# Performance work log

Measured on AMD Instinct MI355X. Metric: run time of the kernel, lower is better.

The kernel has to match this reference:

```python
import jax, jax.numpy as jnp
import numpy as np

WIDTH = 256
HEAD = 16
SCALE = 2
G = WIDTH // HEAD          # 16 groups
NH = G * SCALE             # 32 kernelized heads
EPS = 1e-5
N_NODES = 20000
B_GRAPHS = 1024


def setup_inputs() -> dict:
    key = jax.random.key(0)
    ks = jax.random.split(key, 10)
    x = jax.random.normal(ks[0], (N_NODES, WIDTH), jnp.float32)
    x_res = jax.random.normal(ks[1], (B_GRAPHS, NH, HEAD, HEAD), jnp.float32)
    batch = jnp.sort(jax.random.randint(ks[2], (N_NODES,), 0, B_GRAPHS)).astype(jnp.int64)
    w_pre = jax.random.normal(ks[3], (WIDTH, WIDTH), jnp.float32) * 0.02
    b_pre = jnp.zeros((WIDTH,), jnp.float32)
    # grouped 1x1 convs: [groups, width_scale, head_out, head_in]
    wq = jax.random.normal(ks[4], (G, SCALE, HEAD, HEAD), jnp.float32) * 0.02
    wk = jax.random.normal(ks[5], (G, SCALE, HEAD, HEAD), jnp.float32) * 0.02
    wv = jax.random.normal(ks[6], (G, SCALE, HEAD, HEAD), jnp.float32) * 0.02
    w_post = jax.random.normal(ks[7], (WIDTH, WIDTH * SCALE), jnp.float32) * 0.02
    b_post = jnp.zeros((WIDTH,), jnp.float32)
    log_scale = jnp.full((WIDTH,), np.log(0.01), jnp.float32)
    return {"x": x, "x_res": x_res, "batch": batch, "batch_size": B_GRAPHS,
            "w_pre": w_pre, "b_pre": b_pre, "wq": wq, "wk": wk, "wv": wv,
            "w_post": w_post, "b_post": b_post, "log_scale": log_scale}


def reference(x, x_res, batch, batch_size, w_pre, b_pre, wq, wk, wv, w_post, b_post, log_scale):
    n = x.shape[0]
    # pre: 1x1 conv (= linear) + GroupNorm(affine=False); L=1 so normalize over
    # each group's width_head channels.
    y = x @ w_pre.T + b_pre                       # [N, width]
    yg = y.reshape(n, G, HEAD)                    # [N, G, Hd]
    mu = yg.mean(-1, keepdims=True)
    var = yg.var(-1, keepdims=True)               # biased, as in GroupNorm
    yn = (yg - mu) / jnp.sqrt(var + EPS)          # [N, G, Hd]

    inv_sqrt_h = 1.0 / np.sqrt(HEAD)
    # grouped convs -> kernelized q,k (exp) and v
    xq = jnp.exp(jnp.einsum('ngi,gsoi->ngso', yn, wq) * inv_sqrt_h).reshape(n, NH, HEAD)
    xk = jnp.exp(jnp.einsum('ngi,gsoi->ngso', yn, wk) * inv_sqrt_h).reshape(n, NH, HEAD)
    xv = jnp.einsum('ngi,gsoi->ngso', yn, wv).reshape(n, NH, HEAD)

    # outer product k (x) v then scatter-sum over graphs  [B, NH, Hd, Hd]
    kv = jnp.einsum('bnh,bnv->bnhv', xk, xv)
    kv_sum = jax.ops.segment_sum(kv, batch, num_segments=batch_size) + x_res
    x_res_out = kv_sum

    # per-graph key sum, gathered back to nodes
    k_sum = jax.ops.segment_sum(xk, batch, num_segments=batch_size)[batch]  # [N, NH, Hd]
    denom = jnp.einsum('bnh,bnh->bn', xq, k_sum)                            # [N, NH]
    qn = xq / denom[:, :, None]

    out = jnp.einsum('bnh,bnhv->bnv', qn, kv_sum[batch]).reshape(n, WIDTH * SCALE)
    out = jnp.exp(log_scale) * (out @ w_post.T + b_post)                    # [N, width]
    return (out, x_res_out)
```

## Files before the change

kernel.cpp:

```cpp
#include <hip/hip_runtime.h>
#include <stdint.h>

typedef unsigned int u32;
typedef unsigned short u16;
typedef __attribute__((ext_vector_type(8))) short v8s;
typedef __attribute__((ext_vector_type(4))) float v4f;

#define GN_EPS 1e-5f

__device__ __forceinline__ float bflo(u32 u){ return __uint_as_float(u << 16); }
__device__ __forceinline__ float bfhi(u32 u){ return __uint_as_float(u & 0xffff0000u); }
__device__ __forceinline__ u16 f2bf(float f){
  u32 x = __float_as_uint(f);
  u32 r = (x + 0x7fffu + ((x >> 16) & 1u)) >> 16;
  return (u16)r;
}
__device__ __forceinline__ u32 pack2(float a, float b){
  return (u32)f2bf(a) | ((u32)f2bf(b) << 16);
}
__device__ __forceinline__ void unpack8(const uint4 u, float* f){
  f[0]=bflo(u.x); f[1]=bfhi(u.x); f[2]=bflo(u.y); f[3]=bfhi(u.y);
  f[4]=bflo(u.z); f[5]=bfhi(u.z); f[6]=bflo(u.w); f[7]=bfhi(u.w);
}
__device__ __forceinline__ uint4 loadpack8(const float* __restrict__ p){
  float4 a = *(const float4*)p, b = *(const float4*)(p + 4);
  return make_uint4(pack2(a.x,a.y),pack2(a.z,a.w),pack2(b.x,b.y),pack2(b.z,b.w));
}

__device__ __forceinline__ int getb(const int* __restrict__ b, int is64, int i){
  return b[is64 ? 2*i : i];
}

__global__ __launch_bounds__(256) void k_detect(
    const int* __restrict__ batch, int n, int* __restrict__ flags)
{
  int i = blockIdx.x*256 + threadIdx.x;
  int bad = 0;
  if (i < n - 1 && batch[i] > batch[i + 1]) bad = 1;
  if (__builtin_amdgcn_ballot_w64(bad) != 0 && (threadIdx.x & 63) == 0)
    atomicOr(&flags[0], 1);
}

__global__ __launch_bounds__(256) void k_pre(
    const float* __restrict__ x, const float* __restrict__ wpre,
    const float* __restrict__ bpre, float* __restrict__ y, int N, int nbm)
{
  __shared__ __align__(16) u16 As[64*40];
  __shared__ __align__(16) u16 Bs[64*40];
  const int t = threadIdx.x;
  const int bm = blockIdx.x % nbm;
  const int bn = blockIdx.x / nbm;
  const int m_base = bm*64, n_base = bn*64;
  const int w = t >> 6, lane = t & 63;
  const int wm = (w >> 1)*32, wn = (w & 1)*32;
  const int fr = lane & 15, fk = lane >> 4;
  const int srow = t >> 2, scol = (t & 3)*8;

  v4f acc[2][2];
#pragma unroll
  for (int i = 0; i < 2; i++)
#pragma unroll
    for (int j = 0; j < 2; j++) acc[i][j] = (v4f){0.f,0.f,0.f,0.f};

  for (int k0 = 0; k0 < 256; k0 += 32) {
    __syncthreads();
    {
      int gm = m_base + srow;
      uint4 av = make_uint4(0u,0u,0u,0u);
      if (gm < N) av = loadpack8(x + (size_t)gm*256 + k0 + scol);
      *(uint4*)&As[srow*40 + scol] = av;
      uint4 bv = loadpack8(wpre + (size_t)(n_base + srow)*256 + k0 + scol);
      *(uint4*)&Bs[srow*40 + scol] = bv;
    }
    __syncthreads();
    v8s a0 = *(const v8s*)&As[(wm      + fr)*40 + fk*8];
    v8s a1 = *(const v8s*)&As[(wm + 16 + fr)*40 + fk*8];
    v8s b0 = *(const v8s*)&Bs[(wn      + fr)*40 + fk*8];
    v8s b1 = *(const v8s*)&Bs[(wn + 16 + fr)*40 + fk*8];
    acc[0][0] = __builtin_amdgcn_mfma_f32_16x16x32_bf16(a0,b0,acc[0][0],0,0,0);
    acc[0][1] = __builtin_amdgcn_mfma_f32_16x16x32_bf16(a0,b1,acc[0][1],0,0,0);
    acc[1][0] = __builtin_amdgcn_mfma_f32_16x16x32_bf16(a1,b0,acc[1][0],0,0,0);
    acc[1][1] = __builtin_amdgcn_mfma_f32_16x16x32_bf16(a1,b1,acc[1][1],0,0,0);
  }
#pragma unroll
  for (int nj = 0; nj < 2; nj++) {
    int col = n_base + wn + nj*16 + fr;
    float bpv = bpre[col];
#pragma unroll
    for (int mi = 0; mi < 2; mi++) {
#pragma unroll
      for (int r = 0; r < 4; r++) {
        int row = m_base + wm + mi*16 + fk*4 + r;
        if (row < N) y[(size_t)row*256 + col] = acc[mi][nj][r] + bpv;
      }
    }
  }
}

__global__ __launch_bounds__(256) void k_gnqkv(
    const float* __restrict__ y, const float* __restrict__ wq,
    const float* __restrict__ wk, const float* __restrict__ wv,
    u16* __restrict__ qo, u16* __restrict__ ko, u16* __restrict__ vo, int N)
{
  __shared__ __align__(16) float wL[3*512];
  const int t = threadIdx.x;
  const int g = blockIdx.x & 15;
  const int c = blockIdx.x >> 4;
  {
    const float* srcs[3] = {wq, wk, wv};
#pragma unroll
    for (int tz = 0; tz < 3; tz++) {
      wL[tz*512 + t]       = srcs[tz][g*512 + t];
      wL[tz*512 + t + 256] = srcs[tz][g*512 + t + 256];
    }
  }
  __syncthreads();
  const int node = c*256 + t;
  if (node >= N) return;

  const float* yp = y + (size_t)node*256 + g*16;
  float4 v0 = *(const float4*)yp;
  float4 v1 = *(const float4*)(yp + 4);
  float4 v2 = *(const float4*)(yp + 8);
  float4 v3 = *(const float4*)(yp + 12);
  float a[16] = {v0.x,v0.y,v0.z,v0.w, v1.x,v1.y,v1.z,v1.w,
                 v2.x,v2.y,v2.z,v2.w, v3.x,v3.y,v3.z,v3.w};
  float mu = 0.f;
#pragma unroll
  for (int i = 0; i < 16; i++) mu += a[i];
  mu *= 0.0625f;
  float s2 = 0.f;
#pragma unroll
  for (int i = 0; i < 16; i++) { float d = a[i]-mu; s2 = fmaf(d,d,s2); }
  float inv = rsqrtf(s2*0.0625f + GN_EPS);
  float yn[16];
#pragma unroll
  for (int i = 0; i < 16; i++) yn[i] = (a[i]-mu)*inv;

  u16* outs[3] = {qo, ko, vo};
#pragma unroll
  for (int tz = 0; tz < 3; tz++) {
#pragma unroll
    for (int s = 0; s < 2; s++) {
      u32 p[8];
#pragma unroll
      for (int o = 0; o < 16; o++) {
        const float* row = &wL[tz*512 + (s*16 + o)*16];
        float4 W0 = *(const float4*)row;
        float4 W1 = *(const float4*)(row + 4);
        float4 W2 = *(const float4*)(row + 8);
        float4 W3 = *(const float4*)(row + 12);
        float w[16] = {W0.x,W0.y,W0.z,W0.w,W1.x,W1.y,W1.z,W1.w,
                       W2.x,W2.y,W2.z,W2.w,W3.x,W3.y,W3.z,W3.w};
        float d = 0.f;
#pragma unroll
        for (int i = 0; i < 16; i++) d = fmaf(yn[i], w[i], d);
        if (tz < 2) d = __expf(d*0.25f);
        if (o & 1) p[o>>1] |= (u32)f2bf(d) << 16;
        else       p[o>>1]  = (u32)f2bf(d);
      }
      u16* dst = outs[tz] + (size_t)node*512 + g*32 + s*16;
      *(uint4*)dst       = make_uint4(p[0],p[1],p[2],p[3]);
      *(uint4*)(dst + 8) = make_uint4(p[4],p[5],p[6],p[7]);
    }
  }
}

__device__ __forceinline__ int lbound(const int* __restrict__ a, int is64,
                                      int lo, int n, int key){
  int l = lo, h = n;
  while (l < h) { int m = (l + h) >> 1; if (getb(a, is64, m) < key) l = m + 1; else h = m; }
  return l;
}

__global__ __launch_bounds__(256) void k_segatt(
    const u16* __restrict__ xk, const u16* __restrict__ xv,
    const u16* __restrict__ xq, const float* __restrict__ xres,
    const int* __restrict__ batch, const int* __restrict__ flags,
    float* __restrict__ out1, u16* __restrict__ att, int N)
{
  __shared__ float ksh[4][512];
  __shared__ float vsh[4][512];
  __shared__ __align__(16) float kvs[32*258];
  __shared__ __align__(16) float kss[32*17];
  const int b = blockIdx.x, t = threadIdx.x;
  const int is64 = flags[0];
  const int lo = lbound(batch, is64, 0, N, b);
  const int hi = lbound(batch, is64, lo, N, b + 1);

  float kv[2][16];
#pragma unroll
  for (int r = 0; r < 2; r++)
#pragma unroll
    for (int v = 0; v < 16; v++) kv[r][v] = 0.f;
  float ks0 = 0.f, ks1 = 0.f;
  const int nh = t >> 3, hp = t & 7;

  for (int base = lo; base < hi; base += 4) {
    __syncthreads();
    {
      int j = t >> 6, e8 = (t & 63)*8;
      uint4 K4 = make_uint4(0u,0u,0u,0u), V4 = make_uint4(0u,0u,0u,0u);
      int node = base + j;
      if (node < hi) {
        K4 = *(const uint4*)(xk + (size_t)node*512 + e8);
        V4 = *(const uint4*)(xv + (size_t)node*512 + e8);
      }
      float kf[8], vf[8]; unpack8(K4, kf); unpack8(V4, vf);
#pragma unroll
      for (int i = 0; i < 8; i++) { ksh[j][e8+i] = kf[i]; vsh[j][e8+i] = vf[i]; }
    }
    __syncthreads();
#pragma unroll
    for (int j = 0; j < 4; j++) {
      float k0 = ksh[j][nh*16 + 2*hp], k1 = ksh[j][nh*16 + 2*hp + 1];
      float4 V0 = *(const float4*)&vsh[j][nh*16];
      float4 V1 = *(const float4*)&vsh[j][nh*16 + 4];
      float4 V2 = *(const float4*)&vsh[j][nh*16 + 8];
      float4 V3 = *(const float4*)&vsh[j][nh*16 + 12];
      float vv[16] = {V0.x,V0.y,V0.z,V0.w,V1.x,V1.y,V1.z,V1.w,
                      V2.x,V2.y,V2.z,V2.w,V3.x,V3.y,V3.z,V3.w};
#pragma unroll
      for (int v = 0; v < 16; v++) {
        kv[0][v] = fmaf(k0, vv[v], kv[0][v]);
        kv[1][v] = fmaf(k1, vv[v], kv[1][v]);
      }
      ks0 += ksh[j][2*t]; ks1 += ksh[j][2*t + 1];
    }
  }
  kss[nh*17 + 2*hp]     = ks0;
  kss[nh*17 + 2*hp + 1] = ks1;

#pragma unroll
  for (int r = 0; r < 2; r++) {
    int h = 2*hp + r;
    size_t idx = ((size_t)(b*32 + nh)*16 + h)*16;
    const float* xp = xres + idx;
    float4 X0 = *(const float4*)xp;
    float4 X1 = *(const float4*)(xp + 4);
    float4 X2 = *(const float4*)(xp + 8);
    float4 X3 = *(const float4*)(xp + 12);
    float xf[16] = {X0.x,X0.y,X0.z,X0.w,X1.x,X1.y,X1.z,X1.w,
                    X2.x,X2.y,X2.z,X2.w,X3.x,X3.y,X3.z,X3.w};
    float o[16];
#pragma unroll
    for (int j = 0; j < 16; j++) o[j] = kv[r][j] + xf[j];
    float* op = out1 + idx;
    *(float4*)op        = make_float4(o[0],o[1],o[2],o[3]);
    *(float4*)(op + 4)  = make_float4(o[4],o[5],o[6],o[7]);
    *(float4*)(op + 8)  = make_float4(o[8],o[9],o[10],o[11]);
    *(float4*)(op + 12) = make_float4(o[12],o[13],o[14],o[15]);
    float* lp = &kvs[nh*258 + h*16];
#pragma unroll
    for (int j = 0; j < 8; j++)
      *(float2*)&lp[2*j] = make_float2(o[2*j], o[2*j+1]);
  }
  __syncthreads();

  const int nh2 = t & 31, ns = t >> 5;
  for (int n0 = lo; n0 < hi; n0 += 8) {
    int node = n0 + ns;
    if (node >= hi) continue;
    const u16* qp = xq + (size_t)node*512 + nh2*16;
    uint4 Q0 = *(const uint4*)qp;
    uint4 Q1 = *(const uint4*)(qp + 8);
    float q[16]; unpack8(Q0, q); unpack8(Q1, q + 8);
    const float* ksp = &kss[nh2*17];
    float denom = 0.f;
#pragma unroll
    for (int i = 0; i < 16; i++) denom = fmaf(q[i], ksp[i], denom);
    float inv = 1.0f / fmaxf(denom, 1e-20f);
    float a[16];
#pragma unroll
    for (int v = 0; v < 16; v++) a[v] = 0.f;
    const float* kvp = &kvs[nh2*258];
#pragma unroll
    for (int h = 0; h < 16; h++) {
      float qh = q[h] * inv;
#pragma unroll
      for (int j = 0; j < 8; j++) {
        float2 w = *(const float2*)&kvp[h*16 + 2*j];
        a[2*j]   = fmaf(qh, w.x, a[2*j]);
        a[2*j+1] = fmaf(qh, w.y, a[2*j+1]);
      }
    }
    u32 p[8];
#pragma unroll
    for (int j = 0; j < 8; j++) p[j] = pack2(a[2*j], a[2*j+1]);
    u16* dst = att + (size_t)node*512 + nh2*16;
    *(uint4*)dst       = make_uint4(p[0],p[1],p[2],p[3]);
    *(uint4*)(dst + 8) = make_uint4(p[4],p[5],p[6],p[7]);
  }
}

__global__ __launch_bounds__(256) void k_post(
    const u16* __restrict__ att, const float* __restrict__ wpost,
    const float* __restrict__ bpost, const float* __restrict__ ls,
    float* __restrict__ out0, int N, int nbm)
{
  __shared__ __align__(16) u16 As[64*40];
  __shared__ __align__(16) u16 Bs[64*40];
  const int t = threadIdx.x;
  const int bm = blockIdx.x % nbm;
  const int bn = blockIdx.x / nbm;
  const int m_base = bm*64, n_base = bn*64;
  const int w = t >> 6, lane = t & 63;
  const int wm = (w >> 1)*32, wn = (w & 1)*32;
  const int fr = lane & 15, fk = lane >> 4;
  const int srow = t >> 2, scol = (t & 3)*8;

  v4f acc[2][2];
#pragma unroll
  for (int i = 0; i < 2; i++)
#pragma unroll
    for (int j = 0; j < 2; j++) acc[i][j] = (v4f){0.f,0.f,0.f,0.f};

  for (int k0 = 0; k0 < 512; k0 += 32) {
    __syncthreads();
    {
      int gm = m_base + srow;
      uint4 av = make_uint4(0u,0u,0u,0u);
      if (gm < N) av = *(const uint4*)(att + (size_t)gm*512 + k0 + scol);
      *(uint4*)&As[srow*40 + scol] = av;
      uint4 bv = loadpack8(wpost + (size_t)(n_base + srow)*512 + k0 + scol);
      *(uint4*)&Bs[srow*40 + scol] = bv;
    }
    __syncthreads();
    v8s a0 = *(const v8s*)&As[(wm      + fr)*40 + fk*8];
    v8s a1 = *(const v8s*)&As[(wm + 16 + fr)*40 + fk*8];
    v8s b0 = *(const v8s*)&Bs[(wn      + fr)*40 + fk*8];
    v8s b1 = *(const v8s*)&Bs[(wn + 16 + fr)*40 + fk*8];
    acc[0][0] = __builtin_amdgcn_mfma_f32_16x16x32_bf16(a0,b0,acc[0][0],0,0,0);
    acc[0][1] = __builtin_amdgcn_mfma_f32_16x16x32_bf16(a0,b1,acc[0][1],0,0,0);
    acc[1][0] = __builtin_amdgcn_mfma_f32_16x16x32_bf16(a1,b0,acc[1][0],0,0,0);
    acc[1][1] = __builtin_amdgcn_mfma_f32_16x16x32_bf16(a1,b1,acc[1][1],0,0,0);
  }
#pragma unroll
  for (int nj = 0; nj < 2; nj++) {
    int col = n_base + wn + nj*16 + fr;
    float bpv = bpost[col];
    float e   = __expf(ls[col]);
#pragma unroll
    for (int mi = 0; mi < 2; mi++) {
#pragma unroll
      for (int r = 0; r < 4; r++) {
        int row = m_base + wm + mi*16 + fk*4 + r;
        if (row < N) out0[(size_t)row*256 + col] = e*(acc[mi][nj][r] + bpv);
      }
    }
  }
}

extern "C" void kernel_launch(void* const* d_in, const int* in_sizes, int n_in,
                              void* d_out, int out_size, void* d_ws, size_t ws_size,
                              hipStream_t stream)
{
  const float* x     = (const float*)d_in[0];
  const float* xres  = (const float*)d_in[1];
  const int*   batch = (const int*)d_in[2];
  const float* wpre  = (const float*)d_in[4];
  const float* bpre  = (const float*)d_in[5];
  const float* wq    = (const float*)d_in[6];
  const float* wk    = (const float*)d_in[7];
  const float* wv    = (const float*)d_in[8];
  const float* wpost = (const float*)d_in[9];
  const float* bpost = (const float*)d_in[10];
  const float* ls    = (const float*)d_in[11];

  const int N = in_sizes[0] / 256;
  const int B = in_sizes[1] / 8192;
  const int nbm = (N + 63) / 64;
  const int nchunk = (N + 255) / 256;

  char* ws = (char*)d_ws;
  size_t off = 0;
  int*   flags = (int*)(ws + off); off += 256;
  float* y     = (float*)(ws + off);
  u16*   att   = (u16*)(ws + off);  off += (size_t)N * 1024;
  u16*   q     = (u16*)(ws + off);  off += (size_t)N * 1024;
  u16*   kten  = (u16*)(ws + off);  off += (size_t)N * 1024;
  u16*   vten  = (u16*)(ws + off);  off += (size_t)N * 1024;

  float* out0 = (float*)d_out;
  float* out1 = out0 + (size_t)N * 256;

  hipMemsetAsync(flags, 0, 4, stream);
  k_detect<<<nchunk,         256, 0, stream>>>(batch, N, flags);
  k_pre   <<<nbm * 4,        256, 0, stream>>>(x, wpre, bpre, y, N, nbm);
  k_gnqkv <<<nchunk * 16,    256, 0, stream>>>(y, wq, wk, wv, q, kten, vten, N);
  k_segatt<<<B,              256, 0, stream>>>(kten, vten, q, xres, batch, flags,
                                               out1, att, N);
  k_post  <<<nbm * 4,        256, 0, stream>>>(att, wpost, bpost, ls, out0, N, nbm);
}
```

Before: 138.4 us.

## Precompute segment bounds and stream K/V directly from global in segatt

Adds a kernel that computes per-graph start offsets once, replacing the two binary searches each segatt block ran over the batch array. The K/V accumulation loop drops the LDS staging and per-4-node barriers, so each thread now reads its own K pair and V row straight from global memory, node by node. The combined kv tile held in LDS is stored as bf16 instead of fp32, which cuts LDS footprint and may raise occupancy, but adds rounding to the att computation. It also adds one extra kernel launch, and the direct global loads are redundant across threads, so they rely on cache hits.

Measured after the change: 135.9 us. About the same (-1.8%).

```diff
diff --git a/kernel.cpp b/kernel.cpp
--- a/kernel.cpp
+++ b/kernel.cpp
@@ -39,6 +39,20 @@
   if (i < n - 1 && batch[i] > batch[i + 1]) bad = 1;
   if (__builtin_amdgcn_ballot_w64(bad) != 0 && (threadIdx.x & 63) == 0)
     atomicOr(&flags[0], 1);
+}
+
+__global__ __launch_bounds__(256) void k_bounds(
+    const int* __restrict__ batch, const int* __restrict__ flags,
+    int N, int B, int* __restrict__ bounds)
+{
+  int i = blockIdx.x*256 + threadIdx.x;
+  if (i >= N) return;
+  const int is64 = flags[0];
+  int b = getb(batch, is64, i);
+  int prev = (i == 0) ? -1 : getb(batch, is64, i - 1);
+  for (int g = prev + 1; g <= b; g++) bounds[g] = i;
+  if (i == N - 1)
+    for (int g = b + 1; g <= B; g++) bounds[g] = N;
 }
 
 __global__ __launch_bounds__(256) void k_pre(
@@ -166,27 +180,17 @@
   }
 }
 
-__device__ __forceinline__ int lbound(const int* __restrict__ a, int is64,
-                                      int lo, int n, int key){
-  int l = lo, h = n;
-  while (l < h) { int m = (l + h) >> 1; if (getb(a, is64, m) < key) l = m + 1; else h = m; }
-  return l;
-}
-
 __global__ __launch_bounds__(256) void k_segatt(
     const u16* __restrict__ xk, const u16* __restrict__ xv,
     const u16* __restrict__ xq, const float* __restrict__ xres,
-    const int* __restrict__ batch, const int* __restrict__ flags,
+    const int* __restrict__ bounds,
     float* __restrict__ out1, u16* __restrict__ att, int N)
 {
-  __shared__ float ksh[4][512];
-  __shared__ float vsh[4][512];
-  __shared__ __align__(16) float kvs[32*258];
-  __shared__ __align__(16) float kss[32*17];
+  __shared__ __align__(16) u16 kvs[32*280];
+  __shared__ float kss[32*17];
   const int b = blockIdx.x, t = threadIdx.x;
-  const int is64 = flags[0];
-  const int lo = lbound(batch, is64, 0, N, b);
-  const int hi = lbound(batch, is64, lo, N, b + 1);
+  const int lo = bounds[b], hi = bounds[b+1];
+  const int nh = t >> 3, hp = t & 7;
 
   float kv[2][16];
 #pragma unroll
@@ -194,38 +198,20 @@
 #pragma unroll
     for (int v = 0; v < 16; v++) kv[r][v] = 0.f;
   float ks0 = 0.f, ks1 = 0.f;
-  const int nh = t >> 3, hp = t & 7;
-
-  for (int base = lo; base < hi; base += 4) {
-    __syncthreads();
-    {
-      int j = t >> 6, e8 = (t & 63)*8;
-      uint4 K4 = make_uint4(0u,0u,0u,0u), V4 = make_uint4(0u,0u,0u,0u);
-      int node = base + j;
-      if (node < hi) {
-        K4 = *(const uint4*)(xk + (size_t)node*512 + e8);
-        V4 = *(const uint4*)(xv + (size_t)node*512 + e8);
-      }
-      float kf[8], vf[8]; unpack8(K4, kf); unpack8(V4, vf);
-#pragma unroll
-      for (int i = 0; i < 8; i++) { ksh[j][e8+i] = kf[i]; vsh[j][e8+i] = vf[i]; }
-    }
-    __syncthreads();
-#pragma unroll
-    for (int j = 0; j < 4; j++) {
-      float k0 = ksh[j][nh*16 + 2*hp], k1 = ksh[j][nh*16 + 2*hp + 1];
-      float4 V0 = *(const float4*)&vsh[j][nh*16];
-      float4 V1 = *(const float4*)&vsh[j][nh*16 + 4];
-      float4 V2 = *(const float4*)&vsh[j][nh*16 + 8];
-      float4 V3 = *(const float4*)&vsh[j][nh*16 + 12];
-      float vv[16] = {V0.x,V0.y,V0.z,V0.w,V1.x,V1.y,V1.z,V1.w,
-                      V2.x,V2.y,V2.z,V2.w,V3.x,V3.y,V3.z,V3.w};
-#pragma unroll
-      for (int v = 0; v < 16; v++) {
-        kv[0][v] = fmaf(k0, vv[v], kv[0][v]);
-        kv[1][v] = fmaf(k1, vv[v], kv[1][v]);
-      }
-      ks0 += ksh[j][2*t]; ks1 += ksh[j][2*t + 1];
+
+  const size_t koff = (size_t)nh*16 + 2*hp;
+  const size_t voff = (size_t)nh*16;
+  for (int node = lo; node < hi; node++) {
+    u32 kw = *(const u32*)(xk + (size_t)node*512 + koff);
+    uint4 V0 = *(const uint4*)(xv + (size_t)node*512 + voff);
+    uint4 V1 = *(const uint4*)(xv + (size_t)node*512 + voff + 8);
+    float k0 = bflo(kw), k1 = bfhi(kw);
+    float vf[16]; unpack8(V0, vf); unpack8(V1, vf + 8);
+    ks0 += k0; ks1 += k1;
+#pragma unroll
+    for (int v = 0; v < 16; v++) {
+      kv[0][v] = fmaf(k0, vf[v], kv[0][v]);
+      kv[1][v] = fmaf(k1, vf[v], kv[1][v]);
     }
   }
   kss[nh*17 + 2*hp]     = ks0;
@@ -250,10 +236,11 @@
     *(float4*)(op + 4)  = make_float4(o[4],o[5],o[6],o[7]);
     *(float4*)(op + 8)  = make_float4(o[8],o[9],o[10],o[11]);
     *(float4*)(op + 12) = make_float4(o[12],o[13],o[14],o[15]);
-    float* lp = &kvs[nh*258 + h*16];
-#pragma unroll
-    for (int j = 0; j < 8; j++)
-      *(float2*)&lp[2*j] = make_float2(o[2*j], o[2*j+1]);
+    u16* lp = &kvs[nh*280 + h*16];
+    *(uint4*)lp       = make_uint4(pack2(o[0],o[1]),  pack2(o[2],o[3]),
+                                   pack2(o[4],o[5]),  pack2(o[6],o[7]));
+    *(uint4*)(lp + 8) = make_uint4(pack2(o[8],o[9]),  pack2(o[10],o[11]),
+                                   pack2(o[12],o[13]),pack2(o[14],o[15]));
   }
   __syncthreads();
 
@@ -273,16 +260,15 @@
     float a[16];
 #pragma unroll
     for (int v = 0; v < 16; v++) a[v] = 0.f;
-    const float* kvp = &kvs[nh2*258];
+    const u16* kvp = &kvs[nh2*280];
 #pragma unroll
     for (int h = 0; h < 16; h++) {
       float qh = q[h] * inv;
-#pragma unroll
-      for (int j = 0; j < 8; j++) {
-        float2 w = *(const float2*)&kvp[h*16 + 2*j];
-        a[2*j]   = fmaf(qh, w.x, a[2*j]);
-        a[2*j+1] = fmaf(qh, w.y, a[2*j+1]);
-      }
+      uint4 W0 = *(const uint4*)(kvp + h*16);
+      uint4 W1 = *(const uint4*)(kvp + h*16 + 8);
+      float w[16]; unpack8(W0, w); unpack8(W1, w + 8);
+#pragma unroll
+      for (int v = 0; v < 16; v++) a[v] = fmaf(qh, w[v], a[v]);
     }
     u32 p[8];
 #pragma unroll
@@ -374,21 +360,23 @@
 
   char* ws = (char*)d_ws;
   size_t off = 0;
-  int*   flags = (int*)(ws + off); off += 256;
-  float* y     = (float*)(ws + off);
-  u16*   att   = (u16*)(ws + off);  off += (size_t)N * 1024;
-  u16*   q     = (u16*)(ws + off);  off += (size_t)N * 1024;
-  u16*   kten  = (u16*)(ws + off);  off += (size_t)N * 1024;
-  u16*   vten  = (u16*)(ws + off);  off += (size_t)N * 1024;
+  int*   flags  = (int*)(ws + off); off += 256;
+  int*   bounds = (int*)(ws + off); off += ((size_t)B + 64) * 4;
+  float* y      = (float*)(ws + off);
+  u16*   att    = (u16*)(ws + off);  off += (size_t)N * 1024;
+  u16*   q      = (u16*)(ws + off);  off += (size_t)N * 1024;
+  u16*   kten   = (u16*)(ws + off);  off += (size_t)N * 1024;
+  u16*   vten   = (u16*)(ws + off);  off += (size_t)N * 1024;
 
   float* out0 = (float*)d_out;
   float* out1 = out0 + (size_t)N * 256;
 
   hipMemsetAsync(flags, 0, 4, stream);
   k_detect<<<nchunk,         256, 0, stream>>>(batch, N, flags);
+  k_bounds<<<nchunk,         256, 0, stream>>>(batch, flags, N, B, bounds);
   k_pre   <<<nbm * 4,        256, 0, stream>>>(x, wpre, bpre, y, N, nbm);
   k_gnqkv <<<nchunk * 16,    256, 0, stream>>>(y, wq, wk, wv, q, kten, vten, N);
-  k_segatt<<<B,              256, 0, stream>>>(kten, vten, q, xres, batch, flags,
+  k_segatt<<<B,              256, 0, stream>>>(kten, vten, q, xres, bounds,
                                                out1, att, N);
   k_post  <<<nbm * 4,        256, 0, stream>>>(att, wpost, bpost, ls, out0, N, nbm);
 }
```
